# Performance work log

Hardware: AMD Instinct MI355X
Metric: run time of the kernel (lower is better)

The kernel has to match this reference:

```python
import jax, jax.numpy as jnp
import numpy as np

B, T, C = 4, 2048, 1024
H = 16
DH = C // H  # 64


def setup_inputs() -> dict:
    key = jax.random.key(0)
    ks = jax.random.split(key, 10)
    s_in = 1.0 / np.sqrt(C)
    x = jax.random.normal(ks[0], (B, T, C), dtype=jnp.float32)
    # stacked per-head projection weights: [H, C, DH]
    Wq = jax.random.normal(ks[1], (H, C, DH), dtype=jnp.float32) * s_in
    bq = jnp.zeros((H, DH), dtype=jnp.float32)
    Wk = jax.random.normal(ks[2], (H, C, DH), dtype=jnp.float32) * s_in
    bk = jnp.zeros((H, DH), dtype=jnp.float32)
    Wv = jax.random.normal(ks[3], (H, C, DH), dtype=jnp.float32) * s_in
    bv = jnp.zeros((H, DH), dtype=jnp.float32)
    Wo = jax.random.normal(ks[4], (C, C), dtype=jnp.float32) * s_in
    bo = jnp.zeros((C,), dtype=jnp.float32)
    return {"x": x, "Wq": Wq, "bq": bq, "Wk": Wk, "bk": bk,
            "Wv": Wv, "bv": bv, "Wo": Wo, "bo": bo}


def reference(x, Wq, bq, Wk, bk, Wv, bv, Wo, bo):
    # per-head projections: (B,T,C) x (H,C,DH) -> (B,H,T,DH)
    q = jnp.einsum('btc,hcd->bhtd', x, Wq) + bq[None, :, None, :]
    k = jnp.einsum('btc,hcd->bhtd', x, Wk) + bk[None, :, None, :]
    v = jnp.einsum('btc,hcd->bhtd', x, Wv) + bv[None, :, None, :]
    # scores scaled by C**-0.5 (C = full input embedding dim, as in source)
    scale = jnp.float32(C) ** -0.5
    scores = jnp.einsum('bhtd,bhsd->bhts', q, k) * scale  # (B,H,T,T)
    causal = jnp.tril(jnp.ones((T, T), dtype=bool))
    scores = jnp.where(causal, scores, -jnp.inf)
    attn = jax.nn.softmax(scores, axis=-1)
    out = jnp.einsum('bhts,bhsd->bhtd', attn, v)  # (B,H,T,DH)
    out = out.transpose(0, 2, 1, 3).reshape(B, T, C)  # concat heads
    return out @ Wo + bo
```

## Files before the change

### kernel.cpp

```cpp
#include <hip/hip_runtime.h>
#include <hip/hip_bf16.h>

#define TDIM 2048
#define BDIM 4
#define CDIM 1024
#define HDIM 16
#define DH   64

typedef __hip_bfloat16 bf16;
typedef __attribute__((ext_vector_type(8))) short bf16x8;
typedef __attribute__((ext_vector_type(4))) float f32x4;

__device__ __forceinline__ void async_ld16(const bf16* g, bf16* l) {
    __builtin_amdgcn_global_load_lds(
        (const __attribute__((address_space(1))) unsigned int*)g,
        (__attribute__((address_space(3))) unsigned int*)l, 16, 0, 0);
}

__device__ __forceinline__ unsigned short bf16bits(float x) {
    bf16 b = __float2bfloat16(x);
    return *(unsigned short*)&b;
}

__global__ void convert_x4(const float4* __restrict__ src, ushort4* __restrict__ dst, int n4) {
    int i = blockIdx.x * blockDim.x + threadIdx.x;
    if (i >= n4) return;
    float4 v = src[i];
    ushort4 o;
    o.x = bf16bits(v.x); o.y = bf16bits(v.y);
    o.z = bf16bits(v.z); o.w = bf16bits(v.w);
    dst[i] = o;
}

__global__ void convert_biases(const float* __restrict__ b0, const float* __restrict__ b1,
                               const float* __restrict__ b2, const float* __restrict__ b3,
                               bf16* __restrict__ dst) {
    int i = blockIdx.x * blockDim.x + threadIdx.x;
    int which = i >> 10, j = i & 1023;
    const float* src = (which == 0) ? b0 : (which == 1) ? b1 : (which == 2) ? b2 : b3;
    dst[i] = __float2bfloat16(src[j]);
}

__global__ __launch_bounds__(256) void transpose_qkv_kernel(
    const float* __restrict__ Wq, const float* __restrict__ Wk, const float* __restrict__ Wv,
    bf16* __restrict__ WqT, bf16* __restrict__ WkT, bf16* __restrict__ WvT) {
    __shared__ float tile[64][65];
    const int which = blockIdx.z >> 4, h = blockIdx.z & 15;
    const float* W  = ((which == 0) ? Wq  : (which == 1) ? Wk  : Wv)  + (size_t)h * CDIM * DH;
    bf16*        WT = ((which == 0) ? WqT : (which == 1) ? WkT : WvT) + (size_t)h * CDIM * DH;
    const int c0 = blockIdx.x * 64;
    for (int it = 0; it < 16; it++) {
        int e = it * 256 + threadIdx.x;
        int r = e >> 6, col = e & 63;
        tile[r][col] = W[(size_t)(c0 + r) * DH + col];
    }
    __syncthreads();
    for (int it = 0; it < 16; it++) {
        int e = it * 256 + threadIdx.x;
        int r = e >> 6, col = e & 63;
        WT[(size_t)r * CDIM + c0 + col] = __float2bfloat16(tile[col][r]);
    }
}

__global__ __launch_bounds__(256) void transpose_wo_kernel(
    const float* __restrict__ W, bf16* __restrict__ WT) {
    __shared__ float tile[64][65];
    const int c0 = blockIdx.x * 64, d0 = blockIdx.y * 64;
    for (int it = 0; it < 16; it++) {
        int e = it * 256 + threadIdx.x;
        int r = e >> 6, col = e & 63;
        tile[r][col] = W[(size_t)(c0 + r) * CDIM + d0 + col];
    }
    __syncthreads();
    for (int it = 0; it < 16; it++) {
        int e = it * 256 + threadIdx.x;
        int r = e >> 6, col = e & 63;
        WT[(size_t)(d0 + r) * CDIM + c0 + col] = __float2bfloat16(tile[col][r]);
    }
}

__global__ __launch_bounds__(256) void transpose_v_kernel(
    const bf16* __restrict__ V, bf16* __restrict__ Vt) {
    __shared__ unsigned short tile[64][65];
    const int bh = blockIdx.y, t0 = blockIdx.x * 64;
    const unsigned short* Vp  = (const unsigned short*)V + ((size_t)bh * TDIM + t0) * DH;
    unsigned short*       Vtp = (unsigned short*)Vt + (size_t)bh * DH * TDIM;
    for (int it = 0; it < 16; it++) {
        int e = it * 256 + threadIdx.x;
        int r = e >> 6, c = e & 63;
        tile[r][c] = Vp[(size_t)r * DH + c];
    }
    __syncthreads();
    for (int it = 0; it < 16; it++) {
        int e = it * 256 + threadIdx.x;
        int r = e >> 6, c = e & 63;
        Vtp[(size_t)r * TDIM + t0 + c] = tile[c][r];
    }
}

__global__ __launch_bounds__(256) void proj_qkv_kernel(
    const bf16* __restrict__ X,
    const bf16* __restrict__ WqT, const bf16* __restrict__ WkT, const bf16* __restrict__ WvT,
    const bf16* __restrict__ bq,  const bf16* __restrict__ bk,  const bf16* __restrict__ bvv,
    bf16* __restrict__ Qo, bf16* __restrict__ Ko, bf16* __restrict__ Vo)
{
    const int z = blockIdx.z;
    const bf16* Bt   = (z == 0) ? WqT : (z == 1) ? WkT : WvT;
    const bf16* bias = (z == 0) ? bq  : (z == 1) ? bk  : bvv;

    __shared__ __align__(16) bf16 As[128 * 32];
    __shared__ __align__(16) bf16 Bs[128 * 32];

    const int tid  = threadIdx.x;
    const int lane = tid & 63;
    const int wave = tid >> 6;
    const int wr = wave >> 1, wc = wave & 1;
    const int l15 = lane & 15, quad = lane >> 4;

    const int blockM = blockIdx.y * 128;
    const int blockN = blockIdx.x * 128;

    f32x4 acc[4][4];
    for (int i = 0; i < 4; i++)
        for (int j = 0; j < 4; j++)
            acc[i][j] = (f32x4){0.f, 0.f, 0.f, 0.f};

    const int srow = lane >> 2, scol = (lane & 3) * 8;
    for (int k0 = 0; k0 < CDIM; k0 += 32) {
        for (int cc = 0; cc < 2; cc++) {
            int chunk = wave * 2 + cc;
            int row = chunk * 16 + srow;
            async_ld16(&X [(size_t)(blockM + row) * CDIM + k0 + scol], &As[chunk * 512]);
            async_ld16(&Bt[(size_t)(blockN + row) * CDIM + k0 + scol], &Bs[chunk * 512]);
        }
        __syncthreads();

        bf16x8 af[4], bfr[4];
        for (int mi = 0; mi < 4; mi++)
            af[mi] = *(const bf16x8*)&As[(wr * 64 + mi * 16 + l15) * 32 + quad * 8];
        for (int ni = 0; ni < 4; ni++)
            bfr[ni] = *(const bf16x8*)&Bs[(wc * 64 + ni * 16 + l15) * 32 + quad * 8];

        for (int mi = 0; mi < 4; mi++)
            for (int ni = 0; ni < 4; ni++)
                acc[mi][ni] = __builtin_amdgcn_mfma_f32_16x16x32_bf16(
                    af[mi], bfr[ni], acc[mi][ni], 0, 0, 0);
        __syncthreads();
    }

    for (int mi = 0; mi < 4; mi++) {
        int mbase = blockM + wr * 64 + mi * 16 + quad * 4;
        for (int ni = 0; ni < 4; ni++) {
            int n = blockN + wc * 64 + ni * 16 + l15;
            float bval = __bfloat162float(bias[n]);
            int h = n >> 6, d = n & 63;
            for (int r = 0; r < 4; r++) {
                int mm = mbase + r;
                int b = mm >> 11, t = mm & 2047;
                float val = acc[mi][ni][r] + bval;
                size_t idx = (((size_t)b * HDIM + h) * TDIM + t) * DH + d;
                if (z == 0)      Qo[idx] = __float2bfloat16(val * 0.03125f);
                else if (z == 1) Ko[idx] = __float2bfloat16(val);
                else             Vo[idx] = __float2bfloat16(val);
            }
        }
    }
}

__global__ __launch_bounds__(256) void proj_out_kernel(
    const bf16* __restrict__ X, const bf16* __restrict__ Bt,
    const bf16* __restrict__ bias, float* __restrict__ Out)
{
    __shared__ __align__(16) bf16 As[128 * 32];
    __shared__ __align__(16) bf16 Bs[128 * 32];

    const int tid  = threadIdx.x;
    const int lane = tid & 63;
    const int wave = tid >> 6;
    const int wr = wave >> 1, wc = wave & 1;
    const int l15 = lane & 15, quad = lane >> 4;

    const int blockM = blockIdx.y * 128;
    const int blockN = blockIdx.x * 128;

    f32x4 acc[4][4];
    for (int i = 0; i < 4; i++)
        for (int j = 0; j < 4; j++)
            acc[i][j] = (f32x4){0.f, 0.f, 0.f, 0.f};

    const int srow = lane >> 2, scol = (lane & 3) * 8;
    for (int k0 = 0; k0 < CDIM; k0 += 32) {
        for (int cc = 0; cc < 2; cc++) {
            int chunk = wave * 2 + cc;
            int row = chunk * 16 + srow;
            async_ld16(&X [(size_t)(blockM + row) * CDIM + k0 + scol], &As[chunk * 512]);
            async_ld16(&Bt[(size_t)(blockN + row) * CDIM + k0 + scol], &Bs[chunk * 512]);
        }
        __syncthreads();

        bf16x8 af[4], bfr[4];
        for (int mi = 0; mi < 4; mi++)
            af[mi] = *(const bf16x8*)&As[(wr * 64 + mi * 16 + l15) * 32 + quad * 8];
        for (int ni = 0; ni < 4; ni++)
            bfr[ni] = *(const bf16x8*)&Bs[(wc * 64 + ni * 16 + l15) * 32 + quad * 8];

        for (int mi = 0; mi < 4; mi++)
            for (int ni = 0; ni < 4; ni++)
                acc[mi][ni] = __builtin_amdgcn_mfma_f32_16x16x32_bf16(
                    af[mi], bfr[ni], acc[mi][ni], 0, 0, 0);
        __syncthreads();
    }

    for (int mi = 0; mi < 4; mi++) {
        int mbase = blockM + wr * 64 + mi * 16 + quad * 4;
        for (int ni = 0; ni < 4; ni++) {
            int n = blockN + wc * 64 + ni * 16 + l15;
            float bval = __bfloat162float(bias[n]);
            for (int r = 0; r < 4; r++)
                Out[(size_t)(mbase + r) * CDIM + n] = acc[mi][ni][r] + bval;
        }
    }
}

__global__ __launch_bounds__(256) void attn_kernel(
    const bf16* __restrict__ Q, const bf16* __restrict__ Kb,
    const bf16* __restrict__ Vt, bf16* __restrict__ Y)
{
    const int bh    = blockIdx.y;
    const int qTile = (int)gridDim.x - 1 - blockIdx.x;
    const int qBase = qTile * 64;
    const int tid  = threadIdx.x;
    const int lane = tid & 63, wave = tid >> 6;
    const int l15 = lane & 15, quad = lane >> 4;

    __shared__ __align__(16) bf16 Ks[64 * 80];
    __shared__ __align__(16) bf16 Vs[64 * 80];
    __shared__ __align__(16) bf16 Ps[4][16 * 80];

    const int tq = qBase + wave * 16 + l15;
    bf16x8 qf0 = *(const bf16x8*)&Q[((size_t)bh * TDIM + tq) * DH + quad * 8];
    bf16x8 qf1 = *(const bf16x8*)&Q[((size_t)bh * TDIM + tq) * DH + 32 + quad * 8];

    f32x4 o[4];
    for (int i = 0; i < 4; i++) o[i] = (f32x4){0.f, 0.f, 0.f, 0.f};
    float lsum = 0.f;

    const int r0 = tid >> 3, kc0 = (tid & 7) * 8;

    const int nkt = qTile + 1;
    uint4 kreg0 = *(const uint4*)&Kb[((size_t)bh * TDIM + r0) * DH + kc0];
    uint4 kreg1 = *(const uint4*)&Kb[((size_t)bh * TDIM + r0 + 32) * DH + kc0];
    uint4 vreg0 = *(const uint4*)&Vt[((size_t)bh * DH + r0) * TDIM + kc0];
    uint4 vreg1 = *(const uint4*)&Vt[((size_t)bh * DH + r0 + 32) * TDIM + kc0];

    for (int kt = 0; kt < nkt; kt++) {
        *(uint4*)&Ks[r0 * 80 + kc0]        = kreg0;
        *(uint4*)&Ks[(r0 + 32) * 80 + kc0] = kreg1;
        *(uint4*)&Vs[r0 * 80 + kc0]        = vreg0;
        *(uint4*)&Vs[(r0 + 32) * 80 + kc0] = vreg1;
        __syncthreads();

        if (kt + 1 < nkt) {
            const int nb = (kt + 1) * 64;
            kreg0 = *(const uint4*)&Kb[((size_t)bh * TDIM + nb + r0) * DH + kc0];
            kreg1 = *(const uint4*)&Kb[((size_t)bh * TDIM + nb + r0 + 32) * DH + kc0];
            vreg0 = *(const uint4*)&Vt[((size_t)bh * DH + r0) * TDIM + nb + kc0];
            vreg1 = *(const uint4*)&Vt[((size_t)bh * DH + r0 + 32) * TDIM + nb + kc0];
        }

        f32x4 s[4];
        for (int nt = 0; nt < 4; nt++) {
            bf16x8 k0 = *(const bf16x8*)&Ks[(nt * 16 + l15) * 80 + quad * 8];
            bf16x8 k1 = *(const bf16x8*)&Ks[(nt * 16 + l15) * 80 + 32 + quad * 8];
            f32x4 a = (f32x4){0.f, 0.f, 0.f, 0.f};
            a = __builtin_amdgcn_mfma_f32_16x16x32_bf16(k0, qf0, a, 0, 0, 0);
            a = __builtin_amdgcn_mfma_f32_16x16x32_bf16(k1, qf1, a, 0, 0, 0);
            s[nt] = a;
        }

        const bool diag = (kt == qTile);
        const int qloc = wave * 16 + l15;
        for (int nt = 0; nt < 4; nt++) {
            unsigned short pk[4];
            for (int r = 0; r < 4; r++) {
                float pe = __expf(s[nt][r]);
                if (diag && (nt * 16 + quad * 4 + r > qloc)) pe = 0.f;
                lsum += pe;
                pk[r] = bf16bits(pe);
            }
            *(ushort4*)&Ps[wave][l15 * 80 + nt * 16 + quad * 4] = *(ushort4*)pk;
        }

        bf16x8 pf0 = *(const bf16x8*)&Ps[wave][l15 * 80 + quad * 8];
        bf16x8 pf1 = *(const bf16x8*)&Ps[wave][l15 * 80 + 32 + quad * 8];
        for (int nt = 0; nt < 4; nt++) {
            bf16x8 v0 = *(const bf16x8*)&Vs[(nt * 16 + l15) * 80 + quad * 8];
            bf16x8 v1 = *(const bf16x8*)&Vs[(nt * 16 + l15) * 80 + 32 + quad * 8];
            o[nt] = __builtin_amdgcn_mfma_f32_16x16x32_bf16(v0, pf0, o[nt], 0, 0, 0);
            o[nt] = __builtin_amdgcn_mfma_f32_16x16x32_bf16(v1, pf1, o[nt], 0, 0, 0);
        }
        __syncthreads();
    }

    lsum += __shfl_xor(lsum, 16, 64);
    lsum += __shfl_xor(lsum, 32, 64);
    const float inv = 1.0f / lsum;

    for (int nt = 0; nt < 4; nt++) {
        unsigned short pk[4];
        for (int r = 0; r < 4; r++) pk[r] = bf16bits(o[nt][r] * inv);
        *(ushort4*)&Ps[wave][l15 * 80 + nt * 16 + quad * 4] = *(ushort4*)pk;
    }
    const int b = bh >> 4, h = bh & 15;
    const int qq = lane >> 2, part = lane & 3;
    const int t = qBase + wave * 16 + qq;
    uint4 c0 = *(const uint4*)&Ps[wave][qq * 80 + part * 16];
    uint4 c1 = *(const uint4*)&Ps[wave][qq * 80 + part * 16 + 8];
    *(uint4*)&Y[((size_t)b * TDIM + t) * CDIM + h * DH + part * 16]     = c0;
    *(uint4*)&Y[((size_t)b * TDIM + t) * CDIM + h * DH + part * 16 + 8] = c1;
}

extern "C" void kernel_launch(void* const* d_in, const int* in_sizes, int n_in,
                              void* d_out, int out_size, void* d_ws, size_t ws_size,
                              hipStream_t stream) {
    (void)in_sizes; (void)n_in; (void)out_size; (void)ws_size;

    char* ws = (char*)d_ws;
    const size_t SZ_BHTD = (size_t)BDIM * HDIM * TDIM * DH * sizeof(bf16);
    const size_t SZ_W    = (size_t)HDIM * CDIM * DH * sizeof(bf16);
    bf16* Qb  = (bf16*)(ws);
    bf16* Kb  = (bf16*)(ws + SZ_BHTD);
    bf16* Vt  = (bf16*)(ws + 2 * SZ_BHTD);
    bf16* Y   = (bf16*)(ws + 3 * SZ_BHTD);
    bf16* WqT = (bf16*)(ws + 4 * SZ_BHTD);
    bf16* WkT = (bf16*)(ws + 4 * SZ_BHTD + SZ_W);
    bf16* WvT = (bf16*)(ws + 4 * SZ_BHTD + 2 * SZ_W);
    bf16* WoT = (bf16*)(ws + 4 * SZ_BHTD + 3 * SZ_W);
    bf16* xC  = (bf16*)(ws + 4 * SZ_BHTD + 4 * SZ_W);
    bf16* bqC = (bf16*)(ws + 5 * SZ_BHTD + 4 * SZ_W);
    bf16* bkC = bqC + 1024;
    bf16* bvC = bqC + 2048;
    bf16* boC = bqC + 3072;
    bf16* Vb  = (bf16*)d_out;

    const int nX4 = (BDIM * TDIM * CDIM) / 4;
    convert_x4<<<nX4 / 256, 256, 0, stream>>>((const float4*)d_in[0], (ushort4*)xC, nX4);
    convert_biases<<<16, 256, 0, stream>>>((const float*)d_in[2], (const float*)d_in[4],
                                           (const float*)d_in[6], (const float*)d_in[8], bqC);

    transpose_qkv_kernel<<<dim3(CDIM / 64, 1, 48), 256, 0, stream>>>(
        (const float*)d_in[1], (const float*)d_in[3], (const float*)d_in[5], WqT, WkT, WvT);
    transpose_wo_kernel<<<dim3(CDIM / 64, CDIM / 64), 256, 0, stream>>>(
        (const float*)d_in[7], WoT);

    dim3 gq(CDIM / 128, (BDIM * TDIM) / 128, 3);
    proj_qkv_kernel<<<gq, 256, 0, stream>>>(xC, WqT, WkT, WvT, bqC, bkC, bvC, Qb, Kb, Vb);

    transpose_v_kernel<<<dim3(TDIM / 64, BDIM * HDIM), 256, 0, stream>>>(Vb, Vt);

    attn_kernel<<<dim3(TDIM / 64, BDIM * HDIM), 256, 0, stream>>>(Qb, Kb, Vt, Y);

    proj_out_kernel<<<dim3(CDIM / 128, (BDIM * TDIM) / 128), 256, 0, stream>>>(
        Y, WoT, boC, (float*)d_out);
}
```

Measured before the change: 312.6 us.

## Split attention key tile across waves and reduce partial outputs in shared memory

The attention kernel now has each wave own a 16-key slice of every 64-key tile for all 64 queries, instead of each wave owning 16 queries over all keys. P stays in registers and feeds a 16x16x16 MFMA directly against V, so the per-wave P round trip through shared memory is gone. The cost is a cross-wave reduction of the 64x64 partial output and the row sums through shared memory at the end, with four serialized sync steps. It also raises register pressure, since each wave holds 16 accumulators and Q fragments for all 64 queries.

```diff
diff --git a/kernel.cpp b/kernel.cpp
--- a/kernel.cpp
+++ b/kernel.cpp
@@ -9,6 +9,7 @@
 
 typedef __hip_bfloat16 bf16;
 typedef __attribute__((ext_vector_type(8))) short bf16x8;
+typedef __attribute__((ext_vector_type(4))) short bf16x4;
 typedef __attribute__((ext_vector_type(4))) float f32x4;
 
 __device__ __forceinline__ void async_ld16(const bf16* g, bf16* l) {
@@ -20,6 +21,18 @@
 __device__ __forceinline__ unsigned short bf16bits(float x) {
     bf16 b = __float2bfloat16(x);
     return *(unsigned short*)&b;
+}
+
+__device__ __forceinline__ f32x4 mfma_16x16x16_bf16(bf16x4 a, bf16x4 b, f32x4 c) {
+#if __has_builtin(__builtin_amdgcn_mfma_f32_16x16x16_bf16)
+    return __builtin_amdgcn_mfma_f32_16x16x16_bf16(a, b, c, 0, 0, 0);
+#elif __has_builtin(__builtin_amdgcn_mfma_f32_16x16x16bf16_1k)
+    return __builtin_amdgcn_mfma_f32_16x16x16bf16_1k(a, b, c, 0, 0, 0);
+#else
+    asm volatile("v_mfma_f32_16x16x16_bf16 %0, %1, %2, %0"
+                 : "+v"(c) : "v"(a), "v"(b));
+    return c;
+#endif
 }
 
 __global__ void convert_x4(const float4* __restrict__ src, ushort4* __restrict__ dst, int n4) {
@@ -233,17 +246,24 @@
     const int lane = tid & 63, wave = tid >> 6;
     const int l15 = lane & 15, quad = lane >> 4;
 
-    __shared__ __align__(16) bf16 Ks[64 * 80];
-    __shared__ __align__(16) bf16 Vs[64 * 80];
-    __shared__ __align__(16) bf16 Ps[4][16 * 80];
-
-    const int tq = qBase + wave * 16 + l15;
-    bf16x8 qf0 = *(const bf16x8*)&Q[((size_t)bh * TDIM + tq) * DH + quad * 8];
-    bf16x8 qf1 = *(const bf16x8*)&Q[((size_t)bh * TDIM + tq) * DH + 32 + quad * 8];
-
-    f32x4 o[4];
-    for (int i = 0; i < 4; i++) o[i] = (f32x4){0.f, 0.f, 0.f, 0.f};
-    float lsum = 0.f;
+    __shared__ __align__(16) char smem[2 * 64 * 72 * 2 + 4 * 64 * 4];
+    bf16*  Ks   = (bf16*)smem;
+    bf16*  Vs   = Ks + 64 * 72;
+    float* Of   = (float*)smem;
+    float* dbuf = (float*)(smem + 2 * 64 * 72 * 2);
+
+    bf16x8 qf[4][2];
+    for (int nt = 0; nt < 4; nt++) {
+        const size_t qrow = (size_t)bh * TDIM + qBase + nt * 16 + l15;
+        qf[nt][0] = *(const bf16x8*)&Q[qrow * DH + quad * 8];
+        qf[nt][1] = *(const bf16x8*)&Q[qrow * DH + 32 + quad * 8];
+    }
+
+    f32x4 o[4][4];
+    for (int i = 0; i < 4; i++)
+        for (int j = 0; j < 4; j++)
+            o[i][j] = (f32x4){0.f, 0.f, 0.f, 0.f};
+    float lsum[4] = {0.f, 0.f, 0.f, 0.f};
 
     const int r0 = tid >> 3, kc0 = (tid & 7) * 8;
 
@@ -254,10 +274,10 @@
     uint4 vreg1 = *(const uint4*)&Vt[((size_t)bh * DH + r0 + 32) * TDIM + kc0];
 
     for (int kt = 0; kt < nkt; kt++) {
-        *(uint4*)&Ks[r0 * 80 + kc0]        = kreg0;
-        *(uint4*)&Ks[(r0 + 32) * 80 + kc0] = kreg1;
-        *(uint4*)&Vs[r0 * 80 + kc0]        = vreg0;
-        *(uint4*)&Vs[(r0 + 32) * 80 + kc0] = vreg1;
+        *(uint4*)&Ks[r0 * 72 + kc0]        = kreg0;
+        *(uint4*)&Ks[(r0 + 32) * 72 + kc0] = kreg1;
+        *(uint4*)&Vs[r0 * 72 + kc0]        = vreg0;
+        *(uint4*)&Vs[(r0 + 32) * 72 + kc0] = vreg1;
         __syncthreads();
 
         if (kt + 1 < nkt) {
@@ -268,56 +288,71 @@
             vreg1 = *(const uint4*)&Vt[((size_t)bh * DH + r0 + 32) * TDIM + nb + kc0];
         }
 
+        bf16x8 k0 = *(const bf16x8*)&Ks[(wave * 16 + l15) * 72 + quad * 8];
+        bf16x8 k1 = *(const bf16x8*)&Ks[(wave * 16 + l15) * 72 + 32 + quad * 8];
+        bf16x4 vA[4];
+        for (int mt = 0; mt < 4; mt++)
+            vA[mt] = *(const bf16x4*)&Vs[(mt * 16 + l15) * 72 + wave * 16 + quad * 4];
+
         f32x4 s[4];
         for (int nt = 0; nt < 4; nt++) {
-            bf16x8 k0 = *(const bf16x8*)&Ks[(nt * 16 + l15) * 80 + quad * 8];
-            bf16x8 k1 = *(const bf16x8*)&Ks[(nt * 16 + l15) * 80 + 32 + quad * 8];
             f32x4 a = (f32x4){0.f, 0.f, 0.f, 0.f};
-            a = __builtin_amdgcn_mfma_f32_16x16x32_bf16(k0, qf0, a, 0, 0, 0);
-            a = __builtin_amdgcn_mfma_f32_16x16x32_bf16(k1, qf1, a, 0, 0, 0);
+            a = __builtin_amdgcn_mfma_f32_16x16x32_bf16(k0, qf[nt][0], a, 0, 0, 0);
+            a = __builtin_amdgcn_mfma_f32_16x16x32_bf16(k1, qf[nt][1], a, 0, 0, 0);
             s[nt] = a;
         }
 
         const bool diag = (kt == qTile);
-        const int qloc = wave * 16 + l15;
+        const int keyg = kt * 64 + wave * 16 + quad * 4;
         for (int nt = 0; nt < 4; nt++) {
-            unsigned short pk[4];
+            const int qg = qBase + nt * 16 + l15;
+            bf16x4 pb;
             for (int r = 0; r < 4; r++) {
                 float pe = __expf(s[nt][r]);
-                if (diag && (nt * 16 + quad * 4 + r > qloc)) pe = 0.f;
-                lsum += pe;
-                pk[r] = bf16bits(pe);
+                if (diag && (keyg + r > qg)) pe = 0.f;
+                lsum[nt] += pe;
+                pb[r] = (short)bf16bits(pe);
             }
-            *(ushort4*)&Ps[wave][l15 * 80 + nt * 16 + quad * 4] = *(ushort4*)pk;
-        }
-
-        bf16x8 pf0 = *(const bf16x8*)&Ps[wave][l15 * 80 + quad * 8];
-        bf16x8 pf1 = *(const bf16x8*)&Ps[wave][l15 * 80 + 32 + quad * 8];
-        for (int nt = 0; nt < 4; nt++) {
-            bf16x8 v0 = *(const bf16x8*)&Vs[(nt * 16 + l15) * 80 + quad * 8];
-            bf16x8 v1 = *(const bf16x8*)&Vs[(nt * 16 + l15) * 80 + 32 + quad * 8];
-            o[nt] = __builtin_amdgcn_mfma_f32_16x16x32_bf16(v0, pf0, o[nt], 0, 0, 0);
-            o[nt] = __builtin_amdgcn_mfma_f32_16x16x32_bf16(v1, pf1, o[nt], 0, 0, 0);
-        }
-        __syncthreads();
-    }
-
-    lsum += __shfl_xor(lsum, 16, 64);
-    lsum += __shfl_xor(lsum, 32, 64);
-    const float inv = 1.0f / lsum;
-
+            for (int mt = 0; mt < 4; mt++)
+                o[mt][nt] = mfma_16x16x16_bf16(vA[mt], pb, o[mt][nt]);
+        }
+        __syncthreads();
+    }
+
+    float dsum[4];
     for (int nt = 0; nt < 4; nt++) {
-        unsigned short pk[4];
-        for (int r = 0; r < 4; r++) pk[r] = bf16bits(o[nt][r] * inv);
-        *(ushort4*)&Ps[wave][l15 * 80 + nt * 16 + quad * 4] = *(ushort4*)pk;
-    }
+        float v = lsum[nt];
+        v += __shfl_xor(v, 16, 64);
+        v += __shfl_xor(v, 32, 64);
+        dsum[nt] = v;
+    }
+    if (quad == 0)
+        for (int nt = 0; nt < 4; nt++)
+            dbuf[wave * 64 + nt * 16 + l15] = dsum[nt];
+
+    for (int w = 0; w < 4; w++) {
+        if (wave == w) {
+            for (int mt = 0; mt < 4; mt++)
+                for (int nt = 0; nt < 4; nt++)
+                    for (int r = 0; r < 4; r++) {
+                        int d = mt * 16 + quad * 4 + r, q = nt * 16 + l15;
+                        if (w == 0) Of[d * 68 + q]  = o[mt][nt][r];
+                        else        Of[d * 68 + q] += o[mt][nt][r];
+                    }
+        }
+        __syncthreads();
+    }
+
     const int b = bh >> 4, h = bh & 15;
-    const int qq = lane >> 2, part = lane & 3;
-    const int t = qBase + wave * 16 + qq;
-    uint4 c0 = *(const uint4*)&Ps[wave][qq * 80 + part * 16];
-    uint4 c1 = *(const uint4*)&Ps[wave][qq * 80 + part * 16 + 8];
-    *(uint4*)&Y[((size_t)b * TDIM + t) * CDIM + h * DH + part * 16]     = c0;
-    *(uint4*)&Y[((size_t)b * TDIM + t) * CDIM + h * DH + part * 16 + 8] = c1;
+    const int q = tid >> 2, dc = (tid & 3) * 16;
+    const float inv = 1.0f / (dbuf[q] + dbuf[64 + q] + dbuf[128 + q] + dbuf[192 + q]);
+    for (int c = 0; c < 2; c++) {
+        unsigned short pk[8];
+        for (int j = 0; j < 8; j++)
+            pk[j] = bf16bits(Of[(dc + c * 8 + j) * 68 + q] * inv);
+        *(uint4*)&Y[((size_t)b * TDIM + qBase + q) * CDIM + h * DH + dc + c * 8] =
+            *(uint4*)pk;
+    }
 }
 
 extern "C" void kernel_launch(void* const* d_in, const int* in_sizes, int n_in,
```

Measured after the change: 328.9 us. 5.2% more time.
